# Kernel tuning notes

Measured on AMD Instinct MI355X. Metric: run time of the kernel, lower is better.

Reference implementation:

```python
import jax, jax.numpy as jnp
import numpy as np

B = 1024     # number of graphs
NMAX = 128   # max nodes per graph (sizes alternate 128/64 -> total 98304 nodes)
D = 128      # feature dim == UOTPooling.dim
NUM = 4      # Bregman-ADMM iterations
EPS = 1e-8
NEG = -1e9   # masked log-value


def setup_inputs() -> dict:
    key = jax.random.key(0)
    ks = jax.random.split(key, 6)
    sizes = np.where(np.arange(B) % 2 == 0, 128, 64)
    batch = jnp.asarray(np.repeat(np.arange(B), sizes), dtype=jnp.int32)  # (98304,)
    T = int(sizes.sum())
    x = jax.random.normal(ks[0], (T, D), dtype=jnp.float32)
    W1 = jax.random.normal(ks[1], (2 * D, D), dtype=jnp.float32) / np.sqrt(D)
    W2 = jax.random.normal(ks[2], (1, 2 * D), dtype=jnp.float32) / np.sqrt(2 * D)
    a1_raw = 0.1 * jax.random.normal(ks[3], (1, 1), dtype=jnp.float32)
    a2_raw = 0.1 * jax.random.normal(ks[4], (1, 1), dtype=jnp.float32)
    a3_raw = 0.1 * jax.random.normal(ks[5], (1, 1), dtype=jnp.float32)
    return {"x": x, "batch": batch, "W1": W1, "W2": W2,
            "a1_raw": a1_raw, "a2_raw": a2_raw, "a3_raw": a3_raw}


def _segment_softmax(scores, batch):
    # torch_geometric.utils.softmax over ragged segments, numerically stable
    m = jax.ops.segment_max(scores, batch, num_segments=B)
    e = jnp.exp(scores - m[batch])
    s = jax.ops.segment_sum(e, batch, num_segments=B)
    return e / (s[batch] + 1e-16)


def _to_dense_batch(v, batch):
    # scatter flat (T, ...) node values into dense (B, NMAX, ...) + validity mask
    T = v.shape[0]
    counts = jax.ops.segment_sum(jnp.ones((T,), jnp.int32), batch, num_segments=B)
    starts = jnp.cumsum(counts) - counts
    pos = jnp.arange(T, dtype=jnp.int32) - starts[batch]
    dense = jnp.zeros((B, NMAX) + v.shape[1:], v.dtype).at[batch, pos].set(v)
    mask = jnp.zeros((B, NMAX), dtype=bool).at[batch, pos].set(True)
    return dense, mask


def _uot_badmm(xd, p0, q0, a1, a2, a3, mask3):
    # log-domain Bregman-ADMM for entropic unbalanced OT ("badmm-e").
    # T: (B, N, D); row marginal (sum over D) ~ eta (samples), column marginal
    # (sum over N) ~ mu (dims); eta, mu softly tied to priors q0, p0 via KL.
    log_p0 = jnp.log(p0 + EPS)                       # (B, 1, D)
    log_q0 = jnp.log(q0 + EPS)                       # (B, N, 1)
    log_t = jnp.where(mask3, log_q0 + log_p0, NEG)   # (B, N, D)
    log_s = log_t
    log_mu = log_p0                                   # (B, 1, D)
    log_eta = jnp.where(mask3, log_q0, NEG)           # (B, N, 1)
    z = jnp.zeros_like(log_t)
    z1 = jnp.zeros_like(log_mu)
    z2 = jnp.zeros_like(log_eta)
    for _ in range(NUM):
        # T-update: each valid row of T sums to eta (softmax over feature dim)
        y = (xd - z) / a1 + log_s
        log_t = jnp.where(mask3, log_eta + jax.nn.log_softmax(y, axis=2), NEG)
        # S-update: each column of S sums to mu (masked softmax over node dim)
        y = jnp.where(mask3, z / a1 + log_t, NEG)
        log_s = jnp.where(mask3, log_mu + jax.nn.log_softmax(y, axis=1), NEG)
        # closed-form KL-prox updates of the unbalanced marginals
        log_cs = jax.scipy.special.logsumexp(log_s, axis=1, keepdims=True)  # (B,1,D)
        log_mu = (a1 * log_cs + a2 * log_p0 - z1) / (a1 + a2)
        log_rt = jax.scipy.special.logsumexp(log_t, axis=2, keepdims=True)  # (B,N,1)
        log_eta = jnp.where(mask3, (a1 * log_rt + a3 * log_q0 - z2) / (a1 + a3), NEG)
        # dual ascent
        z = z + a1 * (jnp.exp(log_t) - jnp.exp(log_s))
        z1 = z1 + a1 * (jnp.exp(log_mu) - jnp.exp(log_cs))
        z2 = z2 + a1 * (jnp.exp(log_eta) - jnp.exp(log_rt))
    return jnp.exp(log_t)


def reference(x, batch, W1, W2, a1_raw, a2_raw, a3_raw):
    # attention scores -> segment softmax -> sample-marginal prior q0
    scores = jnp.tanh(x @ W1.T) @ W2.T               # (T, 1)
    q0_flat = _segment_softmax(scores, batch)        # (T, 1)
    xd, mask = _to_dense_batch(x, batch)             # (B, NMAX, D), (B, NMAX)
    q0, _ = _to_dense_batch(q0_flat, batch)          # (B, NMAX, 1)
    mask3 = mask[:, :, None]                         # (B, NMAX, 1)
    p0 = jnp.full((B, 1, D), 1.0 / D, dtype=x.dtype)
    a1 = jax.nn.softplus(a1_raw)[0, 0]
    a2 = jax.nn.softplus(a2_raw)[0, 0]
    a3 = jax.nn.softplus(a3_raw)[0, 0]
    trans = _uot_badmm(xd, p0, q0, a1, a2, a3, mask3)  # (B, NMAX, D)
    frot = D * xd * trans * mask3
    return jnp.sum(frot, axis=1)                     # (B, D)
```

## Files before the change

### kernel.cpp

```cpp
#include <hip/hip_runtime.h>
#include <math.h>

#define NEGC -1000000000.0f

using f32x2 = __attribute__((ext_vector_type(2))) float;
using f32x4 = __attribute__((ext_vector_type(4))) float;
using s16x8 = __attribute__((ext_vector_type(8))) short;

__device__ __forceinline__ float softplusf(float v){ return log1pf(expf(v)); }
__device__ __forceinline__ short f2bf(float f){
  unsigned u = __float_as_uint(f);
  unsigned r = (u + 0x7fffu + ((u >> 16) & 1u)) >> 16;
  return (short)r;
}
__device__ __forceinline__ float red32(float v){ return v + __shfl_xor(v, 32, 64); }
__device__ __forceinline__ float frcp(float v){ return __builtin_amdgcn_rcpf(v); }

__global__ __launch_bounds__(256) void k_pack(const float* __restrict__ W1,
                                              short* __restrict__ wpack,
                                              int* __restrict__ cnt){
  if (blockIdx.x == 0 && threadIdx.x < 2) cnt[threadIdx.x] = 0;
  int gid  = blockIdx.x * 256 + threadIdx.x;
  int lane = gid & 63;
  int ft   = gid >> 6;
  int kt   = ft >> 2;
  int dt   = ft & 3;
  const float* src = W1 + (size_t)(kt * 16 + (lane & 15)) * 128 + dt * 32 + (lane >> 4) * 8;
  short o[8];
#pragma unroll
  for (int e = 0; e < 8; ++e) o[e] = f2bf(src[e]);
  *(s16x8*)(wpack + (size_t)gid * 8) = *(const s16x8*)o;
}

__global__ __launch_bounds__(256) void k_seg(const int* __restrict__ batch,
                                             int* __restrict__ starts, int T, int Bn,
                                             int* __restrict__ cnt,
                                             int* __restrict__ bigs,
                                             int* __restrict__ smalls){
  int t = blockIdx.x * 256 + threadIdx.x;
  if (t > Bn) return;
  int lo = 0, hi = T;
  while (lo < hi){ int mid = (lo + hi) >> 1; if (batch[mid] < t) lo = mid + 1; else hi = mid; }
  if (t == Bn){ starts[Bn] = T; return; }
  starts[t] = lo;
  int lo2 = lo, hi2 = T;
  while (lo2 < hi2){ int mid = (lo2 + hi2) >> 1; if (batch[mid] <= t) lo2 = mid + 1; else hi2 = mid; }
  int nb = lo2 - lo;
  if (nb > 64) bigs[atomicAdd(&cnt[0], 1)] = t;
  else         smalls[atomicAdd(&cnt[1], 1)] = t;
}

__global__ __launch_bounds__(1024)
void k_uot(const float* __restrict__ x,
           const int*   __restrict__ starts,
           const int*   __restrict__ cnt,
           const int*   __restrict__ bigs,
           const int*   __restrict__ smalls,
           const short* __restrict__ wpack,
           const float* __restrict__ W2,
           const float* __restrict__ a1r,
           const float* __restrict__ a2r,
           const float* __restrict__ a3r,
           float* __restrict__ out, int T){
  __shared__ __align__(16) short xs[2 * 64 * 128];
  __shared__ __align__(16) float pbuf[16][164];
  __shared__ float scpart[2][4][64];
  __shared__ float rcsb[2][128];
  __shared__ float lq0s[2][128];
  __shared__ float sred[2][2];

  const int b   = blockIdx.x;
  const int tid = threadIdx.x;
  const int nbig   = cnt[0];
  const int nsmall = cnt[1];

  bool solo; int seg;
  const int half  = tid >> 9;
  const int tid_l = tid & 511;
  if (b < nbig){
    solo = true; seg = bigs[b];
  } else {
    const int i = (b - nbig) * 2 + half;
    solo = false;
    if ((b - nbig) * 2 >= nsmall) return;
    if (i >= nsmall) return;
    seg = smalls[i];
  }

  const int start = starts[seg];
  const int nb    = starts[seg + 1] - start;
  const int hh    = solo ? 0 : half;
  const int tl    = solo ? tid : tid_l;
  const int PL    = solo ? 8 : 4;

  if (nb <= 0){
    if (tl < 128) out[(size_t)seg * 128 + tl] = 0.f;
    return;
  }

  const int n    = tl >> 3;
  const int j    = tl & 7;
  const int wvi  = tid >> 6;
  const int lane = tid & 63;
  const int part = tl & (PL - 1);
  const int col  = tl / PL;
  const int cidx = (col >> 4) * 20 + (col & 15);
  const int wq0  = solo ? 0 : half * 8;
  const int NWh  = solo ? 16 : 8;

  const int u      = tid >> 9;
  const int utid   = tid & 511;
  const int ustart = solo ? (start + u * 64) : start;
#pragma unroll
  for (int itr = 0; itr < 2; ++itr){
    int L  = (itr * 512 + utid) * 8;
    int rr = L >> 7;
    int dc = L & 127;
    int grow = ustart + rr; grow = (grow < T) ? grow : (T - 1);
    const float4 v0 = *(const float4*)(x + (size_t)grow * 128 + dc);
    const float4 v1 = *(const float4*)(x + (size_t)grow * 128 + dc + 4);
    short o[8] = {f2bf(v0.x), f2bf(v0.y), f2bf(v0.z), f2bf(v0.w),
                  f2bf(v1.x), f2bf(v1.y), f2bf(v1.z), f2bf(v1.w)};
    int byte = u * 16384 + rr * 256 + ((dc * 2) ^ ((rr & 7) << 4));
    *(s16x8*)((char*)xs + byte) = *(const s16x8*)o;
  }
  __syncthreads();

  {
    const int lw = wvi & 7;
    const int wm = lw & 1;
    const int wn = lw >> 1;
    f32x4 acc[2][4];
#pragma unroll
    for (int mt = 0; mt < 2; ++mt)
#pragma unroll
      for (int kt = 0; kt < 4; ++kt) acc[mt][kt] = (f32x4){0.f, 0.f, 0.f, 0.f};

    const s16x8* wp = (const s16x8*)wpack;
#pragma unroll
    for (int dt = 0; dt < 4; ++dt){
      s16x8 av[2];
#pragma unroll
      for (int mt = 0; mt < 2; ++mt){
        int arow = wm * 32 + mt * 16 + (lane & 15);
        int byte = u * 16384 + arow * 256 + ((dt * 64 + (lane >> 4) * 16) ^ ((arow & 7) << 4));
        av[mt] = *(const s16x8*)((const char*)xs + byte);
      }
#pragma unroll
      for (int kt = 0; kt < 4; ++kt){
        s16x8 wv = wp[(size_t)((((wn * 4 + kt) * 4 + dt)) << 6) + lane];
#pragma unroll
        for (int mt = 0; mt < 2; ++mt)
          acc[mt][kt] = __builtin_amdgcn_mfma_f32_16x16x32_bf16(av[mt], wv, acc[mt][kt], 0, 0, 0);
      }
    }

    float psum[2][4] = {{0.f,0.f,0.f,0.f},{0.f,0.f,0.f,0.f}};
#pragma unroll
    for (int kt = 0; kt < 4; ++kt){
      const float w2v = W2[(wn * 4 + kt) * 16 + (lane & 15)];
#pragma unroll
      for (int mt = 0; mt < 2; ++mt)
#pragma unroll
        for (int r = 0; r < 4; ++r){
          float e = __expf(2.f * acc[mt][kt][r]);
          psum[mt][r] = fmaf((e - 1.f) * frcp(e + 1.f), w2v, psum[mt][r]);
        }
    }
#pragma unroll
    for (int mt = 0; mt < 2; ++mt)
#pragma unroll
      for (int r = 0; r < 4; ++r){
        float v = psum[mt][r];
        v += __shfl_xor(v, 1, 64); v += __shfl_xor(v, 2, 64);
        v += __shfl_xor(v, 4, 64); v += __shfl_xor(v, 8, 64);
        if ((lane & 15) == 0)
          scpart[u][wn][wm * 32 + mt * 16 + (lane >> 4) * 4 + r] = v;
      }
  }
  __syncthreads();

  if (tl < 128){
    float sc = NEGC;
    if (tl < nb){
      const int ru = solo ? (tl >> 6) : hh;
      const int rl = tl & 63;
      sc = scpart[ru][0][rl] + scpart[ru][1][rl] + scpart[ru][2][rl] + scpart[ru][3][rl];
    }
    lq0s[hh][tl] = sc;
  }
  __syncthreads();

  if ((wvi & 7) == 0 && (!solo || wvi == 0)){
    float v0 = lq0s[hh][lane], v1 = lq0s[hh][lane + 64];
    float m = fmaxf(v0, v1);
#pragma unroll
    for (int msk = 32; msk; msk >>= 1) m = fmaxf(m, __shfl_xor(m, msk, 64));
    float s = __expf(v0 - m) + __expf(v1 - m);
#pragma unroll
    for (int msk = 32; msk; msk >>= 1) s += __shfl_xor(s, msk, 64);
    if (lane == 0){ sred[hh][0] = m; sred[hh][1] = s; }
  }
  __syncthreads();
  const float smax = sred[hh][0];
  const float rden = frcp(sred[hh][1] + 1e-16f);
  if (tl < 128){
    float l = NEGC;
    if (tl < nb) l = __logf(__expf(lq0s[hh][tl] - smax) * rden + 1e-8f);
    lq0s[hh][tl] = l;
  }
  __syncthreads();

  const float a1 = softplusf(a1r[0]);
  const float a2 = softplusf(a2r[0]);
  const float a3 = softplusf(a3r[0]);
  const float inv_a1 = 1.f / a1;
  const float log_p0 = logf(1.0f / 128.0f + 1e-8f);

  float emu_use[3];
  {
    float z1 = 0.f, lp = log_p0;
    emu_use[0] = __expf(log_p0);
#pragma unroll
    for (int i = 1; i < 3; ++i){
      float nm = (a1 * lp + a2 * log_p0 - z1) / (a1 + a2);
      z1 += a1 * (__expf(nm) - __expf(lp));
      emu_use[i] = __expf(nm); lp = nm;
    }
  }
  const float lq0 = lq0s[hh][n];
  float eeta_use[4];
  {
    float z2 = 0.f, lp = lq0;
    eeta_use[0] = __expf(lq0);
#pragma unroll
    for (int i = 1; i < 4; ++i){
      float nm = (a1 * lp + a3 * lq0 - z2) / (a1 + a3);
      z2 += a1 * (__expf(nm) - __expf(lp));
      eeta_use[i] = __expf(nm); lp = nm;
    }
  }

  const bool valid = (n < nb);
  const int  nc    = valid ? n : (nb - 1);
  const float* xp  = x + (size_t)(start + nc) * 128 + j * 16;
  f32x2 EX2[8], PZ2[8], S2[8];
  {
    const float s0 = __expf(lq0 + log_p0);
#pragma unroll
    for (int p = 0; p < 8; p += 2){
      float4 v = *(const float4*)(xp + p * 2);
      EX2[p]   = (f32x2){__expf(v.x * inv_a1), __expf(v.y * inv_a1)};
      EX2[p+1] = (f32x2){__expf(v.z * inv_a1), __expf(v.w * inv_a1)};
    }
#pragma unroll
    for (int p = 0; p < 8; ++p){ PZ2[p] = (f32x2){1.f, 1.f}; S2[p] = (f32x2){s0, s0}; }
  }

#pragma unroll
  for (int it = 0; it < 4; ++it){
    f32x2 ES2[8];
    f32x2 rs2 = (f32x2){0.f, 0.f};
#pragma unroll
    for (int p = 0; p < 8; ++p){
      ES2[p] = EX2[p] * S2[p];
      rs2 += ES2[p] * PZ2[p];
    }
    float rsum = rs2[0] + rs2[1];
    rsum += __shfl_xor(rsum, 1, 64);
    rsum += __shfl_xor(rsum, 2, 64);
    rsum += __shfl_xor(rsum, 4, 64);
    const float Et = valid ? (eeta_use[it] * frcp(rsum)) : 0.f;
    const f32x2 Et2 = (f32x2){Et, Et};

    if (it == 3){
      float c[16];
#pragma unroll
      for (int p = 0; p < 8; p += 2){
        float4 v = *(const float4*)(xp + p * 2);
        f32x2 t0 = ES2[p]   * PZ2[p]   * Et2;
        f32x2 t1 = ES2[p+1] * PZ2[p+1] * Et2;
        c[p*2+0] = v.x * t0[0]; c[p*2+1] = v.y * t0[1];
        c[p*2+2] = v.z * t1[0]; c[p*2+3] = v.w * t1[1];
      }
#pragma unroll
      for (int k = 0; k < 16; ++k){
        float v = red32(c[k]);
        v += __shfl_xor(v, 16, 64);
        v += __shfl_xor(v, 8, 64);
        c[k] = v;
      }
      if (lane < 8){
        float* p = &pbuf[wvi][lane * 20];
        *(float4*)(p + 0)  = make_float4(c[0],  c[1],  c[2],  c[3]);
        *(float4*)(p + 4)  = make_float4(c[4],  c[5],  c[6],  c[7]);
        *(float4*)(p + 8)  = make_float4(c[8],  c[9],  c[10], c[11]);
        *(float4*)(p + 12) = make_float4(c[12], c[13], c[14], c[15]);
      }
      __syncthreads();
      {
        float s = 0.f;
        for (int wq = wq0 + part; wq < wq0 + NWh; wq += PL) s += pbuf[wq][cidx];
        for (int m = 1; m < PL; m <<= 1) s += __shfl_xor(s, m, 64);
        if (part == 0) out[(size_t)seg * 128 + col] = 128.f * s;
      }
    } else {
      const f32x2 Emu2 = (f32x2){emu_use[it], emu_use[it]};
      float c[16];
#pragma unroll
      for (int p = 0; p < 8; ++p){
        f32x2 e2 = ES2[p] * Et2;
        c[p*2+0] = e2[0]; c[p*2+1] = e2[1];
      }
#pragma unroll
      for (int k = 0; k < 16; ++k){
        float v = red32(c[k]);
        v += __shfl_xor(v, 16, 64);
        v += __shfl_xor(v, 8, 64);
        c[k] = v;
      }
      if (lane < 8){
        float* p = &pbuf[wvi][lane * 20];
        *(float4*)(p + 0)  = make_float4(c[0],  c[1],  c[2],  c[3]);
        *(float4*)(p + 4)  = make_float4(c[4],  c[5],  c[6],  c[7]);
        *(float4*)(p + 8)  = make_float4(c[8],  c[9],  c[10], c[11]);
        *(float4*)(p + 12) = make_float4(c[12], c[13], c[14], c[15]);
      }
      __syncthreads();
      {
        float s = 0.f;
        for (int wq = wq0 + part; wq < wq0 + NWh; wq += PL) s += pbuf[wq][cidx];
        for (int m = 1; m < PL; m <<= 1) s += __shfl_xor(s, m, 64);
        if (part == 0) rcsb[hh][col] = frcp(fmaxf(s, 1e-30f));
      }
      __syncthreads();
      f32x2 rc2[8];
      {
        const float4 r0 = *(const float4*)&rcsb[hh][j * 16 + 0];
        const float4 r1 = *(const float4*)&rcsb[hh][j * 16 + 4];
        const float4 r2 = *(const float4*)&rcsb[hh][j * 16 + 8];
        const float4 r3 = *(const float4*)&rcsb[hh][j * 16 + 12];
        rc2[0] = (f32x2){r0.x, r0.y}; rc2[1] = (f32x2){r0.z, r0.w};
        rc2[2] = (f32x2){r1.x, r1.y}; rc2[3] = (f32x2){r1.z, r1.w};
        rc2[4] = (f32x2){r2.x, r2.y}; rc2[5] = (f32x2){r2.z, r2.w};
        rc2[6] = (f32x2){r3.x, r3.y}; rc2[7] = (f32x2){r3.z, r3.w};
      }
#pragma unroll
      for (int p = 0; p < 8; ++p){
        f32x2 e2 = ES2[p] * Et2;
        f32x2 sn = Emu2 * e2 * rc2[p];
        f32x2 arg = sn - e2 * PZ2[p];
        PZ2[p] *= (f32x2){__expf(arg[0]), __expf(arg[1])};
        S2[p] = sn;
      }
    }
  }
}

extern "C" void kernel_launch(void* const* d_in, const int* in_sizes, int n_in,
                              void* d_out, int out_size, void* d_ws, size_t ws_size,
                              hipStream_t stream){
  const float* x    = (const float*)d_in[0];
  const int*   batch= (const int*)  d_in[1];
  const float* W1   = (const float*)d_in[2];
  const float* W2   = (const float*)d_in[3];
  const float* a1r  = (const float*)d_in[4];
  const float* a2r  = (const float*)d_in[5];
  const float* a3r  = (const float*)d_in[6];
  float* out = (float*)d_out;

  const int T  = in_sizes[1];
  const int Bn = out_size / 128;

  short* wpack  = (short*)d_ws;
  int*   starts = (int*)(wpack + 32768);
  int*   cnt    = starts + (Bn + 2);
  int*   bigs   = cnt + 2;
  int*   smalls = bigs + Bn;

  k_pack<<<16, 256, 0, stream>>>(W1, wpack, cnt);
  k_seg<<<(Bn + 256) / 256, 256, 0, stream>>>(batch, starts, T, Bn, cnt, bigs, smalls);
  k_uot<<<Bn, 1024, 0, stream>>>(x, starts, cnt, bigs, smalls, wpack, W2,
                                 a1r, a2r, a3r, out, T);
}
```

Before: 92.17 us.

## Merge prep kernels, use DPP/permlane reductions, drop a sync and fold emu

Merges the weight-packing and segment-search kernels into a single launch, with the counter reset moved to a memset. Replaces several shuffle-xor cross-lane reductions with DPP and permlane swap intrinsics to cut LDS-routed shuffles. Computes each thread's log-prior directly in registers, which removes one block-wide barrier. Folds the mu scale into the stored reciprocal column sums to save multiplies. The memset adds a separate stream operation, and the DPP/permlane paths depend on compiler builtin support.

```diff
diff --git a/kernel.cpp b/kernel.cpp
--- a/kernel.cpp
+++ b/kernel.cpp
@@ -13,41 +13,70 @@
   unsigned r = (u + 0x7fffu + ((u >> 16) & 1u)) >> 16;
   return (short)r;
 }
-__device__ __forceinline__ float red32(float v){ return v + __shfl_xor(v, 32, 64); }
 __device__ __forceinline__ float frcp(float v){ return __builtin_amdgcn_rcpf(v); }
 
-__global__ __launch_bounds__(256) void k_pack(const float* __restrict__ W1,
+__device__ __forceinline__ float addx32(float v){
+#if __has_builtin(__builtin_amdgcn_permlane32_swap)
+  auto r = __builtin_amdgcn_permlane32_swap(__float_as_uint(v), __float_as_uint(v), false, false);
+  return v + __uint_as_float(r[1]);
+#else
+  return v + __shfl_xor(v, 32, 64);
+#endif
+}
+__device__ __forceinline__ float addx16(float v){
+#if __has_builtin(__builtin_amdgcn_permlane16_swap)
+  auto r = __builtin_amdgcn_permlane16_swap(__float_as_uint(v), __float_as_uint(v), false, false);
+  return v + __uint_as_float(r[1]);
+#else
+  return v + __shfl_xor(v, 16, 64);
+#endif
+}
+__device__ __forceinline__ float addx8(float v){
+  int s = __builtin_amdgcn_update_dpp(0, __float_as_int(v), 0x128, 0xF, 0xF, true);
+  return v + __int_as_float(s);
+}
+__device__ __forceinline__ float addq1(float v){
+  int s = __builtin_amdgcn_update_dpp(0, __float_as_int(v), 0xB1, 0xF, 0xF, true);
+  return v + __int_as_float(s);
+}
+__device__ __forceinline__ float addq2(float v){
+  int s = __builtin_amdgcn_update_dpp(0, __float_as_int(v), 0x4E, 0xF, 0xF, true);
+  return v + __int_as_float(s);
+}
+
+__global__ __launch_bounds__(256) void k_prep(const float* __restrict__ W1,
                                               short* __restrict__ wpack,
-                                              int* __restrict__ cnt){
-  if (blockIdx.x == 0 && threadIdx.x < 2) cnt[threadIdx.x] = 0;
-  int gid  = blockIdx.x * 256 + threadIdx.x;
-  int lane = gid & 63;
-  int ft   = gid >> 6;
-  int kt   = ft >> 2;
-  int dt   = ft & 3;
-  const float* src = W1 + (size_t)(kt * 16 + (lane & 15)) * 128 + dt * 32 + (lane >> 4) * 8;
-  short o[8];
-#pragma unroll
-  for (int e = 0; e < 8; ++e) o[e] = f2bf(src[e]);
-  *(s16x8*)(wpack + (size_t)gid * 8) = *(const s16x8*)o;
-}
-
-__global__ __launch_bounds__(256) void k_seg(const int* __restrict__ batch,
-                                             int* __restrict__ starts, int T, int Bn,
-                                             int* __restrict__ cnt,
-                                             int* __restrict__ bigs,
-                                             int* __restrict__ smalls){
-  int t = blockIdx.x * 256 + threadIdx.x;
-  if (t > Bn) return;
-  int lo = 0, hi = T;
-  while (lo < hi){ int mid = (lo + hi) >> 1; if (batch[mid] < t) lo = mid + 1; else hi = mid; }
-  if (t == Bn){ starts[Bn] = T; return; }
-  starts[t] = lo;
-  int lo2 = lo, hi2 = T;
-  while (lo2 < hi2){ int mid = (lo2 + hi2) >> 1; if (batch[mid] <= t) lo2 = mid + 1; else hi2 = mid; }
-  int nb = lo2 - lo;
-  if (nb > 64) bigs[atomicAdd(&cnt[0], 1)] = t;
-  else         smalls[atomicAdd(&cnt[1], 1)] = t;
+                                              const int* __restrict__ batch,
+                                              int* __restrict__ starts, int T, int Bn,
+                                              int* __restrict__ cnt,
+                                              int* __restrict__ bigs,
+                                              int* __restrict__ smalls){
+  const int bx  = blockIdx.x;
+  const int tid = threadIdx.x;
+  if (bx < 16){
+    int gid  = bx * 256 + tid;
+    int lane = gid & 63;
+    int ft   = gid >> 6;
+    int kt   = ft >> 2;
+    int dt   = ft & 3;
+    const float* src = W1 + (size_t)(kt * 16 + (lane & 15)) * 128 + dt * 32 + (lane >> 4) * 8;
+    short o[8];
+#pragma unroll
+    for (int e = 0; e < 8; ++e) o[e] = f2bf(src[e]);
+    *(s16x8*)(wpack + (size_t)gid * 8) = *(const s16x8*)o;
+  } else {
+    int t = (bx - 16) * 256 + tid;
+    if (t > Bn) return;
+    int lo = 0, hi = T;
+    while (lo < hi){ int mid = (lo + hi) >> 1; if (batch[mid] < t) lo = mid + 1; else hi = mid; }
+    if (t == Bn){ starts[Bn] = T; return; }
+    starts[t] = lo;
+    int lo2 = lo, hi2 = T;
+    while (lo2 < hi2){ int mid = (lo2 + hi2) >> 1; if (batch[mid] <= t) lo2 = mid + 1; else hi2 = mid; }
+    int nb = lo2 - lo;
+    if (nb > 64) bigs[atomicAdd(&cnt[0], 1)] = t;
+    else         smalls[atomicAdd(&cnt[1], 1)] = t;
+  }
 }
 
 __global__ __launch_bounds__(1024)
@@ -172,7 +201,7 @@
 #pragma unroll
       for (int r = 0; r < 4; ++r){
         float v = psum[mt][r];
-        v += __shfl_xor(v, 1, 64); v += __shfl_xor(v, 2, 64);
+        v = addq1(v); v = addq2(v);
         v += __shfl_xor(v, 4, 64); v += __shfl_xor(v, 8, 64);
         if ((lane & 15) == 0)
           scpart[u][wn][wm * 32 + mt * 16 + (lane >> 4) * 4 + r] = v;
@@ -204,12 +233,8 @@
   __syncthreads();
   const float smax = sred[hh][0];
   const float rden = frcp(sred[hh][1] + 1e-16f);
-  if (tl < 128){
-    float l = NEGC;
-    if (tl < nb) l = __logf(__expf(lq0s[hh][tl] - smax) * rden + 1e-8f);
-    lq0s[hh][tl] = l;
-  }
-  __syncthreads();
+  const bool  valid = (n < nb);
+  const float lq0 = valid ? __logf(__expf(lq0s[hh][n] - smax) * rden + 1e-8f) : NEGC;
 
   const float a1 = softplusf(a1r[0]);
   const float a2 = softplusf(a2r[0]);
@@ -228,7 +253,6 @@
       emu_use[i] = __expf(nm); lp = nm;
     }
   }
-  const float lq0 = lq0s[hh][n];
   float eeta_use[4];
   {
     float z2 = 0.f, lp = lq0;
@@ -241,7 +265,6 @@
     }
   }
 
-  const bool valid = (n < nb);
   const int  nc    = valid ? n : (nb - 1);
   const float* xp  = x + (size_t)(start + nc) * 128 + j * 16;
   f32x2 EX2[8], PZ2[8], S2[8];
@@ -267,8 +290,8 @@
       rs2 += ES2[p] * PZ2[p];
     }
     float rsum = rs2[0] + rs2[1];
-    rsum += __shfl_xor(rsum, 1, 64);
-    rsum += __shfl_xor(rsum, 2, 64);
+    rsum = addq1(rsum);
+    rsum = addq2(rsum);
     rsum += __shfl_xor(rsum, 4, 64);
     const float Et = valid ? (eeta_use[it] * frcp(rsum)) : 0.f;
     const f32x2 Et2 = (f32x2){Et, Et};
@@ -284,12 +307,8 @@
         c[p*2+2] = v.z * t1[0]; c[p*2+3] = v.w * t1[1];
       }
 #pragma unroll
-      for (int k = 0; k < 16; ++k){
-        float v = red32(c[k]);
-        v += __shfl_xor(v, 16, 64);
-        v += __shfl_xor(v, 8, 64);
-        c[k] = v;
-      }
+      for (int k = 0; k < 16; ++k)
+        c[k] = addx8(addx16(addx32(c[k])));
       if (lane < 8){
         float* p = &pbuf[wvi][lane * 20];
         *(float4*)(p + 0)  = make_float4(c[0],  c[1],  c[2],  c[3]);
@@ -301,11 +320,12 @@
       {
         float s = 0.f;
         for (int wq = wq0 + part; wq < wq0 + NWh; wq += PL) s += pbuf[wq][cidx];
-        for (int m = 1; m < PL; m <<= 1) s += __shfl_xor(s, m, 64);
+        s = addq2(addq1(s));
+        if (PL == 8) s += __shfl_xor(s, 4, 64);
         if (part == 0) out[(size_t)seg * 128 + col] = 128.f * s;
       }
     } else {
-      const f32x2 Emu2 = (f32x2){emu_use[it], emu_use[it]};
+      const float emu = emu_use[it];
       float c[16];
 #pragma unroll
       for (int p = 0; p < 8; ++p){
@@ -313,12 +333,8 @@
         c[p*2+0] = e2[0]; c[p*2+1] = e2[1];
       }
 #pragma unroll
-      for (int k = 0; k < 16; ++k){
-        float v = red32(c[k]);
-        v += __shfl_xor(v, 16, 64);
-        v += __shfl_xor(v, 8, 64);
-        c[k] = v;
-      }
+      for (int k = 0; k < 16; ++k)
+        c[k] = addx8(addx16(addx32(c[k])));
       if (lane < 8){
         float* p = &pbuf[wvi][lane * 20];
         *(float4*)(p + 0)  = make_float4(c[0],  c[1],  c[2],  c[3]);
@@ -330,8 +346,9 @@
       {
         float s = 0.f;
         for (int wq = wq0 + part; wq < wq0 + NWh; wq += PL) s += pbuf[wq][cidx];
-        for (int m = 1; m < PL; m <<= 1) s += __shfl_xor(s, m, 64);
-        if (part == 0) rcsb[hh][col] = frcp(fmaxf(s, 1e-30f));
+        s = addq2(addq1(s));
+        if (PL == 8) s += __shfl_xor(s, 4, 64);
+        if (part == 0) rcsb[hh][col] = emu * frcp(fmaxf(s, 1e-30f));
       }
       __syncthreads();
       f32x2 rc2[8];
@@ -347,9 +364,9 @@
       }
 #pragma unroll
       for (int p = 0; p < 8; ++p){
-        f32x2 e2 = ES2[p] * Et2;
-        f32x2 sn = Emu2 * e2 * rc2[p];
-        f32x2 arg = sn - e2 * PZ2[p];
+        f32x2 e2  = ES2[p] * Et2;
+        f32x2 sn  = e2 * rc2[p];
+        f32x2 arg = e2 * (rc2[p] - PZ2[p]);
         PZ2[p] *= (f32x2){__expf(arg[0]), __expf(arg[1])};
         S2[p] = sn;
       }
@@ -378,8 +395,10 @@
   int*   bigs   = cnt + 2;
   int*   smalls = bigs + Bn;
 
-  k_pack<<<16, 256, 0, stream>>>(W1, wpack, cnt);
-  k_seg<<<(Bn + 256) / 256, 256, 0, stream>>>(batch, starts, T, Bn, cnt, bigs, smalls);
+  hipMemsetAsync(cnt, 0, 2 * sizeof(int), stream);
+  const int segBlocks = (Bn + 256) / 256;
+  k_prep<<<16 + segBlocks, 256, 0, stream>>>(W1, wpack, batch, starts, T, Bn,
+                                             cnt, bigs, smalls);
   k_uot<<<Bn, 1024, 0, stream>>>(x, starts, cnt, bigs, smalls, wpack, W2,
                                  a1r, a2r, a3r, out, T);
 }
```

Measured after the change: 81.86 us. 1.13x faster.
